# Performance work log

Hardware: AMD Instinct MI355X
Metric: run time of the kernel (lower is better)

Reference implementation:

```python
import jax, jax.numpy as jnp
import numpy as np
from functools import partial

B, N, NCLS = 16, 25200, 80
M_TGT = 50
MAX_DET = 300
CONF_THRES = 0.8
NMS_THRES = 0.4


def cxcywh_to_xyxy(boxes):
    # cxcywh -> xywh -> xyxy (as in tensor_to_dict: cxcywh_to_xywh then xywh_to_xyxy)
    cx, cy, w, h = boxes[..., 0], boxes[..., 1], boxes[..., 2], boxes[..., 3]
    x1 = cx - 0.5 * w
    y1 = cy - 0.5 * h
    return jnp.stack([x1, y1, x1 + w, y1 + h], axis=-1)


def pairwise_iou(b):
    # b: [K,4] xyxy
    x1 = jnp.maximum(b[:, None, 0], b[None, :, 0])
    y1 = jnp.maximum(b[:, None, 1], b[None, :, 1])
    x2 = jnp.minimum(b[:, None, 2], b[None, :, 2])
    y2 = jnp.minimum(b[:, None, 3], b[None, :, 3])
    inter = jnp.clip(x2 - x1, 0.0) * jnp.clip(y2 - y1, 0.0)
    area = jnp.clip(b[:, 2] - b[:, 0], 0.0) * jnp.clip(b[:, 3] - b[:, 1], 0.0)
    return inter / (area[:, None] + area[None, :] - inter + 1e-9)


def nms_one(boxes_xyxy, labels, valid):
    # boxes sorted by score descending; class-aware greedy NMS, fixed K iterations
    K = boxes_xyxy.shape[0]
    iou = pairwise_iou(boxes_xyxy)
    same = labels[:, None] == labels[None, :]
    supp = (iou > NMS_THRES) & same
    idx = jnp.arange(K)

    def body(i, keep):
        kill = supp[i] & (idx > i) & keep[i]
        return keep & ~kill

    return jax.lax.fori_loop(0, K, body, valid)


def post_process(preds):
    # preds: [B, N, 5+C] (cx,cy,w,h,obj,cls...)
    obj = preds[..., 4]
    cls_prob = preds[..., 5:]
    cls_conf = jnp.max(cls_prob, axis=-1)
    cls_id = jnp.argmax(cls_prob, axis=-1)
    score = obj * cls_conf                      # [B,N]
    score = jnp.where(score > CONF_THRES, score, 0.0)
    top_s, top_i = jax.lax.top_k(score, MAX_DET)            # [B,K]
    boxes = jnp.take_along_axis(preds[..., :4], top_i[..., None], axis=1)  # cxcywh [B,K,4]
    labels = jnp.take_along_axis(cls_id, top_i, axis=1)     # [B,K]
    valid = top_s > 0.0
    boxes_xyxy = cxcywh_to_xyxy(boxes)
    keep = jax.vmap(nms_one)(boxes_xyxy, labels, valid)     # [B,K]
    scores = jnp.where(keep, top_s, 0.0)
    boxes_xyxy = jnp.where(keep[..., None], boxes_xyxy, 0.0)
    labels = jnp.where(keep, labels, -1)
    return boxes_xyxy, scores, labels, keep


def process_targets(tt, lengths):
    # tt: [B, M, 6] = cxcywh, score, label ; lengths: [B]
    valid = jnp.arange(tt.shape[1])[None, :] < lengths[:, None]  # [B,M]
    boxes = cxcywh_to_xyxy(tt[..., :4])
    scores = tt[..., 4]
    labels = tt[..., 5].astype(jnp.int32)
    boxes = jnp.where(valid[..., None], boxes, 0.0)
    scores = jnp.where(valid, scores, 0.0)
    labels = jnp.where(valid, labels, -1)
    return boxes, scores, labels, valid


def setup_inputs() -> dict:
    key = jax.random.key(0)
    k1, k2, k3, k4 = jax.random.split(key, 4)
    preds = jax.random.uniform(k1, (B, N, 5 + NCLS), dtype=jnp.float32)
    tgt_boxes = jax.random.uniform(k2, (B, M_TGT, 4), dtype=jnp.float32) * 640.0
    tgt_scores = jnp.ones((B, M_TGT, 1), dtype=jnp.float32)
    tgt_labels = jax.random.randint(k3, (B, M_TGT, 1), 0, NCLS).astype(jnp.float32)
    target_target = jnp.concatenate([tgt_boxes, tgt_scores, tgt_labels], axis=-1)
    target_lengths = jax.random.randint(k4, (B,), 1, M_TGT + 1).astype(jnp.int32)
    return {"preds": preds, "target_target": target_target, "target_lengths": target_lengths}


def reference(preds, target_target, target_lengths):
    pb, ps, pl, pv = post_process(preds)
    tb, ts, tl, tv = process_targets(target_target, target_lengths)
    # @torch.no_grad in original forward
    out = (pb, ps, pl, pv, tb, ts, tl, tv)
    return jax.tree_util.tree_map(jax.lax.stop_gradient, out)
```

## Files before the change

### kernel.cpp

```cpp
#include <hip/hip_runtime.h>
#include <cstdint>

#define BB 16
#define NN 25200
#define NCLS 80
#define NF (5 + NCLS)
#define MAXDET 300
#define MTGT 50
#define CONF 0.8f
#define NMSTH 0.4f
#define WORDS 10
#define NBINS 2048
#define CAPALL 8192
#define SBUF 2048
#define APB 64
#define CPB 394
#define SLOTK 48
#define SCORE_BLOCKS (BB * CPB)
#define NTGT_BLOCKS ((BB * MTGT + 127) / 128)
#define HSTRIDE 33

#define WS_CNTS 0
#define WS_KEYS 32768
#define WS_GBOX (WS_KEYS + (size_t)SCORE_BLOCKS * SLOTK * 8)
#define WS_GLAB (WS_GBOX + (size_t)SCORE_BLOCKS * SLOTK * 16)

#define O_PB 0
#define O_PS (BB * MAXDET * 4)
#define O_PL (O_PS + BB * MAXDET)
#define O_PV (O_PL + BB * MAXDET)
#define O_TB (O_PV + BB * MAXDET)
#define O_TS (O_TB + BB * MTGT * 4)
#define O_TL (O_TS + BB * MTGT)
#define O_TV (O_TL + BB * MTGT)

__global__ __launch_bounds__(128) void k_score(const float* __restrict__ preds,
                                               int* __restrict__ cnts,
                                               unsigned long long* __restrict__ keys,
                                               float* __restrict__ gbox,
                                               int* __restrict__ glabel,
                                               const float* __restrict__ tt,
                                               const int* __restrict__ len,
                                               float* __restrict__ out) {
    __shared__ float st[APB * NF];
    __shared__ int wbase0;
    int tid = threadIdx.x;
    int bid = blockIdx.x;

    if (bid >= SCORE_BLOCKS) {
        int t = (bid - SCORE_BLOCKS) * 128 + tid;
        if (t < BB * MTGT) {
            int b = t / MTGT, m = t - b * MTGT;
            const float* row = tt + (size_t)t * 6;
            bool valid = m < len[b];
            float cx = row[0], cy = row[1], w = row[2], h = row[3];
            float x1 = cx - 0.5f * w, y1 = cy - 0.5f * h;
            float* tb = out + O_TB + (size_t)t * 4;
            tb[0] = valid ? x1 : 0.f;
            tb[1] = valid ? y1 : 0.f;
            tb[2] = valid ? (x1 + w) : 0.f;
            tb[3] = valid ? (y1 + h) : 0.f;
            out[O_TS + t] = valid ? row[4] : 0.f;
            out[O_TL + t] = valid ? (float)(int)row[5] : -1.f;
            out[O_TV + t] = valid ? 1.f : 0.f;
        }
        return;
    }

    int b  = bid / CPB;
    int cb = bid - b * CPB;
    int count = (cb == CPB - 1) ? (NN - (CPB - 1) * APB) : APB;
    int nv4 = count * NF / 4;

    int w = tid >> 6;
    int lane = tid & 63;
    const float4* src = (const float4*)(preds + ((size_t)b * NN + (size_t)cb * APB) * NF);
    #pragma unroll
    for (int i = 0; i < 11; ++i) {
        int idx = i * 128 + tid;
        if (idx < nv4) {
            __builtin_amdgcn_global_load_lds(
                (const __attribute__((address_space(1))) void*)(src + idx),
                (__attribute__((address_space(3))) void*)(st + (i * 128 + w * 64) * 4),
                16, 0, 0);
        }
    }
    __syncthreads();

    int a = tid >> 1, h = tid & 1;
    const float* row = st + a * NF;
    const float* cls = row + 5 + h * 40;
    float v0 = cls[0], v1 = cls[1], v2 = cls[2], v3 = cls[3];
    int   i0 = 0,      i1 = 1,      i2 = 2,      i3 = 3;
    #pragma unroll
    for (int f = 4; f < 40; f += 4) {
        if (cls[f]     > v0) { v0 = cls[f];     i0 = f; }
        if (cls[f + 1] > v1) { v1 = cls[f + 1]; i1 = f + 1; }
        if (cls[f + 2] > v2) { v2 = cls[f + 2]; i2 = f + 2; }
        if (cls[f + 3] > v3) { v3 = cls[f + 3]; i3 = f + 3; }
    }
    float v = v0; int ia = i0;
    if (v1 > v || (v1 == v && i1 < ia)) { v = v1; ia = i1; }
    if (v2 > v || (v2 == v && i2 < ia)) { v = v2; ia = i2; }
    if (v3 > v || (v3 == v && i3 < ia)) { v = v3; ia = i3; }
    int ci = h * 40 + ia;
    float ov = __shfl_xor(v, 1);
    int   oi = __shfl_xor(ci, 1);
    if (ov > v || (ov == v && oi < ci)) { v = ov; ci = oi; }
    float s = row[4] * v;

    bool pass = (h == 0) && (a < count) && (s > CONF);
    unsigned long long mask = __ballot(pass);
    int wcnt = __popcll(mask);
    if (w == 0 && lane == 0) wbase0 = wcnt;
    __syncthreads();
    int base = (w == 0) ? 0 : wbase0;
    if (pass) {
        int pos = base + __popcll(mask & ((1ull << lane) - 1ull));
        if (pos < SLOTK) {
            unsigned u = __float_as_uint(s);
            unsigned inv = (unsigned)(NN - 1 - (cb * APB + a));
            unsigned slot = (unsigned)(cb * SLOTK + pos);
            size_t g = (size_t)bid * SLOTK + pos;
            keys[g] = ((unsigned long long)u << 32) |
                      (unsigned long long)((inv << 17) | slot);
            float cx = row[0], cy = row[1], ww = row[2], hh = row[3];
            float x1 = cx - 0.5f * ww, y1 = cy - 0.5f * hh;
            float4 bx = { x1, y1, x1 + ww, y1 + hh };
            ((float4*)gbox)[g] = bx;
            glabel[g] = ci;
        }
    }
    if (w == 1 && lane == 0) {
        int tot = base + wcnt;
        cnts[bid] = tot < SLOTK ? tot : SLOTK;
    }
}

__global__ __launch_bounds__(1024) void k_post(const int* __restrict__ cnts,
                                               const unsigned long long* __restrict__ keys,
                                               const float* __restrict__ gbox,
                                               const int* __restrict__ glabel,
                                               float* __restrict__ out) {
    __shared__ unsigned long long skall[CAPALL];
    __shared__ unsigned long long sk[SBUF];
    __shared__ unsigned long long skTop[MAXDET];
    __shared__ int hist[64 * HSTRIDE];
    __shared__ float4   sbox[MAXDET];
    __shared__ int      slabel[MAXDET];
    __shared__ float    sscore[MAXDET];
    __shared__ unsigned supp[MAXDET * WORDS];
    __shared__ int wsum[16];
    __shared__ int lcnt, lcnt2, scut;
    int b = blockIdx.x;
    int tid = threadIdx.x;
    int lane = tid & 63;
    int wv = tid >> 6;

    if (tid == 0) { lcnt = 0; lcnt2 = 0; }
    for (int i = tid; i < 64 * HSTRIDE; i += 1024) hist[i] = 0;
    if (tid < MAXDET) skTop[tid] = 0ull;
    __syncthreads();

    int c = (tid < CPB) ? cnts[b * CPB + tid] : 0;
    int inc = c;
    #pragma unroll
    for (int d = 1; d < 64; d <<= 1) {
        int o = __shfl_up(inc, d);
        if (lane >= d) inc += o;
    }
    if (lane == 63) wsum[wv] = inc;
    __syncthreads();
    int wbase = 0;
    #pragma unroll
    for (int q = 0; q < 16; ++q) wbase += (q < wv) ? wsum[q] : 0;
    int base = wbase + inc - c;
    if (tid == 1023) lcnt = wbase + inc;
    if (tid < CPB) {
        const unsigned long long* slot = keys + (size_t)(b * CPB + tid) * SLOTK;
        for (int k = 0; k < c; ++k) {
            int p = base + k;
            if (p < CAPALL) skall[p] = slot[k];
        }
    }
    __syncthreads();
    int M = lcnt; if (M > CAPALL) M = CAPALL;
    for (int i = tid; i < M; i += 1024) {
        unsigned u = (unsigned)(skall[i] >> 32);
        int bin = (int)((u - 0x3F400000u) >> 12);
        bin = bin < 0 ? 0 : (bin > NBINS - 1 ? NBINS - 1 : bin);
        atomicAdd(&hist[(bin >> 5) * HSTRIDE + (bin & 31)], 1);
    }
    __syncthreads();

    if (tid < 64) {
        int sb = 0;
        #pragma unroll
        for (int k = 0; k < 32; ++k) sb += hist[lane * HSTRIDE + k];
        int cum = sb;
        #pragma unroll
        for (int d = 1; d < 64; d <<= 1) {
            int o = __shfl_down(cum, d);
            if (lane + d < 64) cum += o;
        }
        unsigned long long m = __ballot(cum >= MAXDET);
        int cutbin = 0;
        if (m) {
            int cutS = 63 - __clzll(m);
            int tail = (cutS < 63) ? __shfl(cum, cutS + 1) : 0;
            int hh = (lane < 32) ? hist[cutS * HSTRIDE + lane] : 0;
            int c2 = hh;
            #pragma unroll
            for (int d = 1; d < 32; d <<= 1) {
                int o = __shfl_down(c2, d);
                if (lane + d < 32) c2 += o;
            }
            c2 += tail;
            unsigned long long m2 = __ballot(lane < 32 && c2 >= MAXDET);
            int cutL = 63 - __clzll(m2);
            cutbin = cutS * 32 + cutL;
        }
        if (lane == 0) scut = cutbin;
    }
    __syncthreads();
    int cutbin = scut;

    for (int i = tid; i < ((M + 1023) & ~1023); i += 1024) {
        bool pass = false;
        unsigned long long key = 0ull;
        if (i < M) {
            key = skall[i];
            unsigned u = (unsigned)(key >> 32);
            int bin = (int)((u - 0x3F400000u) >> 12);
            bin = bin < 0 ? 0 : (bin > NBINS - 1 ? NBINS - 1 : bin);
            pass = bin >= cutbin;
        }
        unsigned long long mask = __ballot(pass);
        int wcnt = __popcll(mask);
        int bs = 0;
        if (lane == 0 && wcnt) bs = atomicAdd(&lcnt2, wcnt);
        bs = __shfl(bs, 0);
        if (pass) {
            int pos = bs + __popcll(mask & ((1ull << lane) - 1ull));
            if (pos < SBUF) sk[pos] = key;
        }
    }
    __syncthreads();

    int M2 = lcnt2; if (M2 > SBUF) M2 = SBUF;
    for (int c2 = tid; c2 < M2; c2 += 1024) {
        unsigned long long key = sk[c2];
        int rank = 0;
        for (int j = 0; j < M2; ++j) rank += (sk[j] > key) ? 1 : 0;
        if (rank < MAXDET) skTop[rank] = key;
    }
    __syncthreads();

    if (tid < MAXDET) {
        unsigned long long key = skTop[tid];
        unsigned sbits = (unsigned)(key >> 32);
        if (sbits) {
            size_t g = (size_t)b * (CPB * SLOTK) + (size_t)(key & 0x1FFFFull);
            sbox[tid]   = ((const float4*)gbox)[g];
            slabel[tid] = glabel[g];
            sscore[tid] = __uint_as_float(sbits);
        } else {
            float4 zz = { 0.f, 0.f, 0.f, 0.f };
            sbox[tid] = zz; slabel[tid] = -1; sscore[tid] = 0.f;
        }
    }
    __syncthreads();

    for (int T = tid; T < MAXDET * WORDS; T += 1024) {
        int i  = T / WORDS;
        int jw = T - i * WORDS;
        unsigned word = 0;
        int jbase = jw * 32;
        if (jbase + 31 > i) {
            float4 bi = sbox[i];
            int   li = slabel[i];
            float si = sscore[i];
            float ai = __fmul_rn(fmaxf(__fsub_rn(bi.z, bi.x), 0.f),
                                 fmaxf(__fsub_rn(bi.w, bi.y), 0.f));
            for (int uu = 0; uu < 32; ++uu) {
                int t = (uu + jw) & 31;
                int j = jbase + t;
                if (j > i && j < MAXDET) {
                    if (slabel[j] == li && si > 0.f && sscore[j] > 0.f) {
                        float4 bj = sbox[j];
                        float xx1 = fmaxf(bi.x, bj.x);
                        float yy1 = fmaxf(bi.y, bj.y);
                        float xx2 = fminf(bi.z, bj.z);
                        float yy2 = fminf(bi.w, bj.w);
                        float iw = fmaxf(__fsub_rn(xx2, xx1), 0.f);
                        float ih = fmaxf(__fsub_rn(yy2, yy1), 0.f);
                        float inter = __fmul_rn(iw, ih);
                        float aj = __fmul_rn(fmaxf(__fsub_rn(bj.z, bj.x), 0.f),
                                             fmaxf(__fsub_rn(bj.w, bj.y), 0.f));
                        float den = __fadd_rn(__fsub_rn(__fadd_rn(ai, aj), inter), 1e-9f);
                        float iou = inter / den;
                        if (iou > NMSTH) word |= 1u << t;
                    }
                }
            }
        }
        supp[T] = word;
    }
    __syncthreads();

    if (tid < 64) {
        unsigned keep = 0, nzm = 0;
        #pragma unroll
        for (int s = 0; s < 5; ++s) {
            int k = s * 64 + lane;
            bool kb = (k < MAXDET) && (sscore[k] > 0.f);
            unsigned long long m = __ballot(kb);
            if (lane == 2 * s)     keep = (unsigned)m;
            if (lane == 2 * s + 1) keep = (unsigned)(m >> 32);
            unsigned nz = 0;
            if (k < MAXDET) {
                #pragma unroll
                for (int w = 0; w < WORDS; ++w) nz |= supp[k * WORDS + w];
            }
            unsigned long long mn = __ballot(nz != 0u);
            if (lane == 2 * s)     nzm = (unsigned)mn;
            if (lane == 2 * s + 1) nzm = (unsigned)(mn >> 32);
        }

        for (int i = 0; i < MAXDET; ++i) {
            int idx = i >> 5;
            unsigned kw = __shfl(keep, idx);
            unsigned nw = __shfl(nzm, idx);
            if (((kw & nw) >> (i & 31)) & 1u) {
                if (lane < WORDS) keep &= ~supp[i * WORDS + lane];
            }
        }

        #pragma unroll
        for (int s = 0; s < 5; ++s) {
            int k = s * 64 + lane;
            if (k < MAXDET) {
                unsigned kw = __shfl(keep, k >> 5);
                bool kp = (kw >> (k & 31)) & 1u;
                int g = b * MAXDET + k;
                float4 bx = sbox[k];
                float4 zz = { 0.f, 0.f, 0.f, 0.f };
                ((float4*)(out + O_PB))[g] = kp ? bx : zz;
                out[O_PS + g] = kp ? sscore[k] : 0.f;
                out[O_PL + g] = kp ? (float)slabel[k] : -1.f;
                out[O_PV + g] = kp ? 1.f : 0.f;
            }
        }
    }
}

extern "C" void kernel_launch(void* const* d_in, const int* in_sizes, int n_in,
                              void* d_out, int out_size, void* d_ws, size_t ws_size,
                              hipStream_t stream) {
    const float* preds = (const float*)d_in[0];
    const float* tt    = (const float*)d_in[1];
    const int*   len   = (const int*)d_in[2];
    float* out = (float*)d_out;

    char* ws = (char*)d_ws;
    int* cnts = (int*)(ws + WS_CNTS);
    unsigned long long* keys = (unsigned long long*)(ws + WS_KEYS);
    float* gbox = (float*)(ws + WS_GBOX);
    int* glabel = (int*)(ws + WS_GLAB);

    k_score<<<SCORE_BLOCKS + NTGT_BLOCKS, 128, 0, stream>>>(preds, cnts, keys, gbox, glabel, tt, len, out);
    k_post <<<BB, 1024, 0, stream>>>(cnts, keys, gbox, glabel, out);
}
```

Measured before the change: 78.27 us.

## Split post-processing into select, suppression-mask and finalize kernels

The per-image post kernel is split into three launches. k_sel picks the top detections and writes them to workspace. k_mask builds the IoU suppression bitmask across many small blocks instead of 16 large ones, and k_fin runs the greedy keep scan. The goal is to spread the pairwise IoU work over more compute units than the 16 blocks used before. In exchange it adds two kernel launches and a round trip of the boxes and masks through global memory, plus unroll pragmas on the rank and IoU loops.

```diff
diff --git a/kernel.cpp b/kernel.cpp
--- a/kernel.cpp
+++ b/kernel.cpp
@@ -24,6 +24,10 @@
 #define WS_KEYS 32768
 #define WS_GBOX (WS_KEYS + (size_t)SCORE_BLOCKS * SLOTK * 8)
 #define WS_GLAB (WS_GBOX + (size_t)SCORE_BLOCKS * SLOTK * 16)
+#define WS_DBOX (WS_GLAB + (size_t)SCORE_BLOCKS * SLOTK * 4)
+#define WS_DLAB (WS_DBOX + (size_t)BB * MAXDET * 16)
+#define WS_DSC  (WS_DLAB + (size_t)BB * MAXDET * 4)
+#define WS_SUPP (WS_DSC + (size_t)BB * MAXDET * 4)
 
 #define O_PB 0
 #define O_PS (BB * MAXDET * 4)
@@ -137,19 +141,17 @@
     }
 }
 
-__global__ __launch_bounds__(1024) void k_post(const int* __restrict__ cnts,
-                                               const unsigned long long* __restrict__ keys,
-                                               const float* __restrict__ gbox,
-                                               const int* __restrict__ glabel,
-                                               float* __restrict__ out) {
+__global__ __launch_bounds__(1024) void k_sel(const int* __restrict__ cnts,
+                                              const unsigned long long* __restrict__ keys,
+                                              const float* __restrict__ gbox,
+                                              const int* __restrict__ glabel,
+                                              float* __restrict__ dbox,
+                                              int* __restrict__ dlab,
+                                              float* __restrict__ dsc) {
     __shared__ unsigned long long skall[CAPALL];
     __shared__ unsigned long long sk[SBUF];
     __shared__ unsigned long long skTop[MAXDET];
     __shared__ int hist[64 * HSTRIDE];
-    __shared__ float4   sbox[MAXDET];
-    __shared__ int      slabel[MAXDET];
-    __shared__ float    sscore[MAXDET];
-    __shared__ unsigned supp[MAXDET * WORDS];
     __shared__ int wsum[16];
     __shared__ int lcnt, lcnt2, scut;
     int b = blockIdx.x;
@@ -251,6 +253,7 @@
     for (int c2 = tid; c2 < M2; c2 += 1024) {
         unsigned long long key = sk[c2];
         int rank = 0;
+        #pragma unroll 4
         for (int j = 0; j < M2; ++j) rank += (sk[j] > key) ? 1 : 0;
         if (rank < MAXDET) skTop[rank] = key;
     }
@@ -259,52 +262,86 @@
     if (tid < MAXDET) {
         unsigned long long key = skTop[tid];
         unsigned sbits = (unsigned)(key >> 32);
+        int g = b * MAXDET + tid;
         if (sbits) {
-            size_t g = (size_t)b * (CPB * SLOTK) + (size_t)(key & 0x1FFFFull);
-            sbox[tid]   = ((const float4*)gbox)[g];
-            slabel[tid] = glabel[g];
-            sscore[tid] = __uint_as_float(sbits);
+            size_t src = (size_t)b * (CPB * SLOTK) + (size_t)(key & 0x1FFFFull);
+            ((float4*)dbox)[g] = ((const float4*)gbox)[src];
+            dlab[g] = glabel[src];
+            dsc[g]  = __uint_as_float(sbits);
         } else {
             float4 zz = { 0.f, 0.f, 0.f, 0.f };
-            sbox[tid] = zz; slabel[tid] = -1; sscore[tid] = 0.f;
-        }
-    }
-    __syncthreads();
-
-    for (int T = tid; T < MAXDET * WORDS; T += 1024) {
-        int i  = T / WORDS;
-        int jw = T - i * WORDS;
-        unsigned word = 0;
-        int jbase = jw * 32;
-        if (jbase + 31 > i) {
-            float4 bi = sbox[i];
-            int   li = slabel[i];
-            float si = sscore[i];
-            float ai = __fmul_rn(fmaxf(__fsub_rn(bi.z, bi.x), 0.f),
-                                 fmaxf(__fsub_rn(bi.w, bi.y), 0.f));
-            for (int uu = 0; uu < 32; ++uu) {
-                int t = (uu + jw) & 31;
-                int j = jbase + t;
-                if (j > i && j < MAXDET) {
-                    if (slabel[j] == li && si > 0.f && sscore[j] > 0.f) {
-                        float4 bj = sbox[j];
-                        float xx1 = fmaxf(bi.x, bj.x);
-                        float yy1 = fmaxf(bi.y, bj.y);
-                        float xx2 = fminf(bi.z, bj.z);
-                        float yy2 = fminf(bi.w, bj.w);
-                        float iw = fmaxf(__fsub_rn(xx2, xx1), 0.f);
-                        float ih = fmaxf(__fsub_rn(yy2, yy1), 0.f);
-                        float inter = __fmul_rn(iw, ih);
-                        float aj = __fmul_rn(fmaxf(__fsub_rn(bj.z, bj.x), 0.f),
-                                             fmaxf(__fsub_rn(bj.w, bj.y), 0.f));
-                        float den = __fadd_rn(__fsub_rn(__fadd_rn(ai, aj), inter), 1e-9f);
-                        float iou = inter / den;
-                        if (iou > NMSTH) word |= 1u << t;
-                    }
+            ((float4*)dbox)[g] = zz;
+            dlab[g] = -1;
+            dsc[g]  = 0.f;
+        }
+    }
+}
+
+__global__ __launch_bounds__(256) void k_mask(const float* __restrict__ dbox,
+                                              const int* __restrict__ dlab,
+                                              const float* __restrict__ dsc,
+                                              unsigned* __restrict__ gsupp) {
+    int T = blockIdx.x * 256 + threadIdx.x;
+    if (T >= BB * MAXDET * WORDS) return;
+    int g  = T / WORDS;
+    int jw = T - g * WORDS;
+    int b  = g / MAXDET;
+    int i  = g - b * MAXDET;
+
+    unsigned word = 0;
+    int jbase = jw * 32;
+    if (jbase + 31 > i) {
+        float4 bi = ((const float4*)dbox)[g];
+        int   li = dlab[g];
+        float si = dsc[g];
+        float ai = __fmul_rn(fmaxf(__fsub_rn(bi.z, bi.x), 0.f),
+                             fmaxf(__fsub_rn(bi.w, bi.y), 0.f));
+        #pragma unroll 4
+        for (int t = 0; t < 32; ++t) {
+            int j = jbase + t;
+            if (j > i && j < MAXDET) {
+                int gj = b * MAXDET + j;
+                if (dlab[gj] == li && si > 0.f && dsc[gj] > 0.f) {
+                    float4 bj = ((const float4*)dbox)[gj];
+                    float xx1 = fmaxf(bi.x, bj.x);
+                    float yy1 = fmaxf(bi.y, bj.y);
+                    float xx2 = fminf(bi.z, bj.z);
+                    float yy2 = fminf(bi.w, bj.w);
+                    float iw = fmaxf(__fsub_rn(xx2, xx1), 0.f);
+                    float ih = fmaxf(__fsub_rn(yy2, yy1), 0.f);
+                    float inter = __fmul_rn(iw, ih);
+                    float aj = __fmul_rn(fmaxf(__fsub_rn(bj.z, bj.x), 0.f),
+                                         fmaxf(__fsub_rn(bj.w, bj.y), 0.f));
+                    float den = __fadd_rn(__fsub_rn(__fadd_rn(ai, aj), inter), 1e-9f);
+                    float iou = inter / den;
+                    if (iou > NMSTH) word |= 1u << t;
                 }
             }
         }
-        supp[T] = word;
+    }
+    gsupp[T] = word;
+}
+
+__global__ __launch_bounds__(1024) void k_fin(const float* __restrict__ dbox,
+                                              const int* __restrict__ dlab,
+                                              const float* __restrict__ dsc,
+                                              const unsigned* __restrict__ gsupp,
+                                              float* __restrict__ out) {
+    __shared__ unsigned ls[MAXDET * WORDS];
+    __shared__ float4   sbox[MAXDET];
+    __shared__ int      slabel[MAXDET];
+    __shared__ float    sscore[MAXDET];
+    int b = blockIdx.x;
+    int tid = threadIdx.x;
+    int lane = tid & 63;
+
+    for (int w = tid; w < MAXDET * WORDS; w += 1024)
+        ls[w] = gsupp[b * MAXDET * WORDS + w];
+    if (tid < MAXDET) {
+        int g = b * MAXDET + tid;
+        sbox[tid]   = ((const float4*)dbox)[g];
+        slabel[tid] = dlab[g];
+        sscore[tid] = dsc[g];
     }
     __syncthreads();
 
@@ -320,7 +357,7 @@
             unsigned nz = 0;
             if (k < MAXDET) {
                 #pragma unroll
-                for (int w = 0; w < WORDS; ++w) nz |= supp[k * WORDS + w];
+                for (int w = 0; w < WORDS; ++w) nz |= ls[k * WORDS + w];
             }
             unsigned long long mn = __ballot(nz != 0u);
             if (lane == 2 * s)     nzm = (unsigned)mn;
@@ -332,7 +369,7 @@
             unsigned kw = __shfl(keep, idx);
             unsigned nw = __shfl(nzm, idx);
             if (((kw & nw) >> (i & 31)) & 1u) {
-                if (lane < WORDS) keep &= ~supp[i * WORDS + lane];
+                if (lane < WORDS) keep &= ~ls[i * WORDS + lane];
             }
         }
 
@@ -365,9 +402,15 @@
     char* ws = (char*)d_ws;
     int* cnts = (int*)(ws + WS_CNTS);
     unsigned long long* keys = (unsigned long long*)(ws + WS_KEYS);
-    float* gbox = (float*)(ws + WS_GBOX);
-    int* glabel = (int*)(ws + WS_GLAB);
+    float* gbox  = (float*)(ws + WS_GBOX);
+    int*   glabel = (int*)(ws + WS_GLAB);
+    float* dbox  = (float*)(ws + WS_DBOX);
+    int*   dlab  = (int*)(ws + WS_DLAB);
+    float* dsc   = (float*)(ws + WS_DSC);
+    unsigned* gsupp = (unsigned*)(ws + WS_SUPP);
 
     k_score<<<SCORE_BLOCKS + NTGT_BLOCKS, 128, 0, stream>>>(preds, cnts, keys, gbox, glabel, tt, len, out);
-    k_post <<<BB, 1024, 0, stream>>>(cnts, keys, gbox, glabel, out);
+    k_sel  <<<BB, 1024, 0, stream>>>(cnts, keys, gbox, glabel, dbox, dlab, dsc);
+    k_mask <<<(BB * MAXDET * WORDS + 255) / 256, 256, 0, stream>>>(dbox, dlab, dsc, gsupp);
+    k_fin  <<<BB, 1024, 0, stream>>>(dbox, dlab, dsc, gsupp, out);
 }
```

Measured after the change: 80.38 us. 1.03x slower.
